# Kernel tuning notes

Measured on AMD Instinct MI355X. Metric: run time of the kernel, lower is better.

Reference implementation:

```python
import jax, jax.numpy as jnp
import numpy as np

K = 128          # num_clusters (init kwarg k)
N_ITERS = 100    # torch loop runs up to 100 iters; converged centroids are a
                 # fixed point, so running all 100 matches the early-exit result


def _sq_dists(x, c):
    # squared Euclidean distances [N, K]; argmin identical to torch.cdist argmin
    return (jnp.sum(x * x, axis=1, keepdims=True)
            - 2.0 * (x @ c.T)
            + jnp.sum(c * c, axis=1)[None, :])


def _assign_and_update(x, c):
    ids = jnp.argmin(_sq_dists(x, c), axis=1)                     # [N]
    sums = jax.ops.segment_sum(x, ids, num_segments=K)            # [K, D]
    counts = jax.ops.segment_sum(jnp.ones((x.shape[0],), x.dtype), ids,
                                 num_segments=K)                  # [K]
    return ids, sums / counts[:, None]   # mean per cluster (NaN if empty, as in torch)


def setup_inputs() -> dict:
    key = jax.random.key(0)
    kx, kp = jax.random.split(key)
    N, D = 32768, 256
    x = jax.random.normal(kx, (N, D), dtype=jnp.float32)
    # torch.randperm(N)[:K] -> distinct initial centroid indices
    init_idx = jax.random.permutation(kp, N)[:K].astype(jnp.int32)
    return {"x": x, "init_idx": init_idx}


def reference(x, init_idx):
    c0 = x[init_idx]  # [K, D]

    def body(c, _):
        _, newc = _assign_and_update(x, c)
        return newc, None

    # 99 updates, then final assignment + update: returned ids correspond to the
    # centroids BEFORE the last update, exactly like the torch loop's last iter.
    c, _ = jax.lax.scan(body, c0, None, length=N_ITERS - 1)
    ids, c = _assign_and_update(x, c)

    logits = x @ c.T  # temperature = 1.0
    logp = jax.nn.log_softmax(logits, axis=-1)
    # CrossEntropyLoss(mean) with pseudo labels = cluster ids
    loss = -jnp.mean(jnp.take_along_axis(logp, ids[:, None], axis=1))
    return loss
```

## Files before the change

kernel.cpp:

```cpp
#include <hip/hip_runtime.h>
#include <cstdint>

#define NPTS 32768
#define DIM  256
#define NK   128
#define NITER 100
#define NBLK 256
#define NTHR 1024
#define PAD  33

typedef unsigned short ushort_t;
typedef unsigned long long ull_t;
typedef __attribute__((ext_vector_type(8))) short s8v;
typedef __attribute__((ext_vector_type(4))) float f4v;

__device__ __forceinline__ unsigned short f2bf(float f) {
  unsigned u = __float_as_uint(f);
  u += 0x7fffu + ((u >> 16) & 1u);
  return (unsigned short)(u >> 16);
}
__device__ __forceinline__ float bf2f(unsigned short b) {
  return __uint_as_float(((unsigned)b) << 16);
}

__device__ __forceinline__ void cstore(float* p, float v) {
  __hip_atomic_store(p, v, __ATOMIC_RELAXED, __HIP_MEMORY_SCOPE_AGENT);
}
__device__ __forceinline__ float cload(const float* p) {
  return __hip_atomic_load(p, __ATOMIC_RELAXED, __HIP_MEMORY_SCOPE_AGENT);
}
__device__ __forceinline__ void cstorei(int* p, int v) {
  __hip_atomic_store(p, v, __ATOMIC_RELAXED, __HIP_MEMORY_SCOPE_AGENT);
}
__device__ __forceinline__ int cloadi(const int* p) {
  return __hip_atomic_load(p, __ATOMIC_RELAXED, __HIP_MEMORY_SCOPE_AGENT);
}
__device__ __forceinline__ void cstore64(ull_t* p, ull_t v) {
  __hip_atomic_store(p, v, __ATOMIC_RELAXED, __HIP_MEMORY_SCOPE_AGENT);
}
__device__ __forceinline__ f4v cload128f(const ull_t* p) {
  ull_t a = __hip_atomic_load(p, __ATOMIC_RELAXED, __HIP_MEMORY_SCOPE_AGENT);
  ull_t b = __hip_atomic_load(p + 1, __ATOMIC_RELAXED, __HIP_MEMORY_SCOPE_AGENT);
  f4v r;
  r[0] = __uint_as_float((unsigned)a); r[1] = __uint_as_float((unsigned)(a >> 32));
  r[2] = __uint_as_float((unsigned)b); r[3] = __uint_as_float((unsigned)(b >> 32));
  return r;
}

__device__ __forceinline__ void gbar(unsigned* flags, unsigned* grep, unsigned gen, bool inv) {
  __syncthreads();
  if (threadIdx.x == 0)
    __hip_atomic_store(&flags[blockIdx.x * 16], gen, __ATOMIC_RELAXED, __HIP_MEMORY_SCOPE_AGENT);
  if (blockIdx.x == 0) {
    if (threadIdx.x < NBLK) {
      while (__hip_atomic_load(&flags[threadIdx.x * 16], __ATOMIC_RELAXED, __HIP_MEMORY_SCOPE_AGENT) < gen)
        __builtin_amdgcn_s_sleep(2);
    }
    __syncthreads();
    if (threadIdx.x < 64)
      __hip_atomic_store(&grep[threadIdx.x * 16], gen, __ATOMIC_RELAXED, __HIP_MEMORY_SCOPE_AGENT);
  }
  if (threadIdx.x == 0) {
    while (__hip_atomic_load(&grep[(blockIdx.x & 63) * 16], __ATOMIC_RELAXED, __HIP_MEMORY_SCOPE_AGENT) < gen)
      __builtin_amdgcn_s_sleep(2);
  }
  __syncthreads();
  if (inv && threadIdx.x == 0) __threadfence();
  asm volatile("" ::: "memory");
  __syncthreads();
}

union StU {
  struct { char ch[128 * 80]; char cl[128 * 80]; } a;
  struct { float accB[NK * PAD]; ushort_t idsl16[1024]; } b;
  struct { float red4[1024]; float redcn[1024]; } c;
};

__device__ __forceinline__ void gemm_core(
    const s8v* __restrict__ xhR, const s8v* __restrict__ xlR,
    StU& u, float* cns, int t,
    const ull_t* __restrict__ cpk, const float* __restrict__ cn2, f4v (&acc)[2][2]) {
  const int lane = t & 63;
  const int w    = t >> 6;
  const int wr   = w >> 2, wc = w & 3;
  const int g    = lane >> 4, lr = lane & 15;

  if (t < NK) cns[t] = cload(&cn2[2 * t]) + cload(&cn2[2 * t + 1]);

  const f4v zero = {0.f, 0.f, 0.f, 0.f};
#pragma unroll
  for (int i = 0; i < 2; ++i)
#pragma unroll
    for (int j = 0; j < 2; ++j) acc[i][j] = zero;

  for (int q = 0; q < 8; ++q) {
    if (t < 512) {
      int row = t >> 2, c = t & 3;
      const ull_t* src = cpk + (size_t)row * 128 + q * 16 + c * 4;
      ull_t w0 = src[0], w1 = src[1], w2 = src[2], w3 = src[3];
      s8v vh, vl;
      vh[0] = (short)w0; vl[0] = (short)(w0 >> 16); vh[1] = (short)(w0 >> 32); vl[1] = (short)(w0 >> 48);
      vh[2] = (short)w1; vl[2] = (short)(w1 >> 16); vh[3] = (short)(w1 >> 32); vl[3] = (short)(w1 >> 48);
      vh[4] = (short)w2; vl[4] = (short)(w2 >> 16); vh[5] = (short)(w2 >> 32); vl[5] = (short)(w2 >> 48);
      vh[6] = (short)w3; vl[6] = (short)(w3 >> 16); vh[7] = (short)(w3 >> 32); vl[7] = (short)(w3 >> 48);
      *(s8v*)(u.a.ch + row * 80 + c * 16) = vh;
      *(s8v*)(u.a.cl + row * 80 + c * 16) = vl;
    }
    __syncthreads();
    s8v ah[2], al[2], bh[2], bl[2];
#pragma unroll
    for (int i = 0; i < 2; ++i) {
      int ra = wr * 32 + i * 16 + lr;
      int o = ra * 512 + (((q * 4 + g) ^ (lr & 7)) * 16);
      ah[i] = *(const s8v*)((const char*)xhR + o);
      al[i] = *(const s8v*)((const char*)xlR + o);
    }
#pragma unroll
    for (int j = 0; j < 2; ++j) {
      int rb = wc * 32 + j * 16 + lr;
      int o = rb * 80 + g * 16;
      bh[j] = *(const s8v*)(u.a.ch + o);
      bl[j] = *(const s8v*)(u.a.cl + o);
    }
#pragma unroll
    for (int i = 0; i < 2; ++i)
#pragma unroll
      for (int j = 0; j < 2; ++j) {
        acc[i][j] = __builtin_amdgcn_mfma_f32_16x16x32_bf16(ah[i], bh[j], acc[i][j], 0, 0, 0);
        acc[i][j] = __builtin_amdgcn_mfma_f32_16x16x32_bf16(ah[i], bl[j], acc[i][j], 0, 0, 0);
        acc[i][j] = __builtin_amdgcn_mfma_f32_16x16x32_bf16(al[i], bh[j], acc[i][j], 0, 0, 0);
      }
    __syncthreads();
  }
}

__global__ __launch_bounds__(NTHR, 1) void kmeans_fused(
    const float* __restrict__ x, const int* __restrict__ init_idx,
    ull_t* __restrict__ cpk, float* __restrict__ cn2, int* __restrict__ ids,
    float* __restrict__ psum, float* __restrict__ pcnt,
    float* __restrict__ outp, unsigned* __restrict__ flags,
    unsigned* __restrict__ grep, float* __restrict__ out) {
  __shared__ s8v xhR[4096];
  __shared__ s8v xlR[4096];
  __shared__ StU u;
  __shared__ float cns[NK];
  __shared__ float redd[NK * 4];
  __shared__ int   redk[NK * 4];
  __shared__ float gmaxs[NK];
  __shared__ float labvs[NK];
  __shared__ int   labis[NK];
  __shared__ int   cntB[NK];
  __shared__ ushort_t hsm[DIM], lsm[DIM];
  __shared__ float cntsh;

  const int b = blockIdx.x;
  const int t = threadIdx.x;
  const int lane = t & 63;
  const int w  = t >> 6;
  const int wr = w >> 2, wc = w & 3;
  const int g  = lane >> 4, lr = lane & 15;
  const int pbase = b * 128;
  unsigned gen = 1;

  for (int i = 0; i < 4; ++i) {
    int G = i * NTHR + t;
    int row = G >> 5, c = G & 31;
    const float4* src = (const float4*)(x + ((size_t)pbase + row) * DIM + c * 8);
    float4 fa = src[0], fb = src[1];
    float vv[8] = {fa.x, fa.y, fa.z, fa.w, fb.x, fb.y, fb.z, fb.w};
    s8v vh, vl;
#pragma unroll
    for (int j = 0; j < 8; ++j) {
      unsigned short hh = f2bf(vv[j]);
      vh[j] = (short)hh;
      vl[j] = (short)f2bf(vv[j] - bf2f(hh));
    }
    int pos = c ^ (row & 7);
    *(s8v*)((char*)xhR + row * 512 + pos * 16) = vh;
    *(s8v*)((char*)xlR + row * 512 + pos * 16) = vl;
  }

  if (b < NK) {
    float eff = 0.f;
    if (t < DIM) {
      float v = x[init_idx[b] * DIM + t];
      unsigned short hh = f2bf(v);
      unsigned short ll = f2bf(v - bf2f(hh));
      hsm[t] = hh; lsm[t] = ll;
      eff = bf2f(hh) + bf2f(ll);
    }
    __syncthreads();
    u.c.redcn[t] = (t < DIM) ? eff * eff : 0.f;
    if (t < NK) {
      ull_t wv = (ull_t)hsm[2 * t] | ((ull_t)lsm[2 * t] << 16)
               | ((ull_t)hsm[2 * t + 1] << 32) | ((ull_t)lsm[2 * t + 1] << 48);
      cstore64(&cpk[(size_t)b * 128 + t], wv);
    }
    __syncthreads();
    for (int s = 512; s > 0; s >>= 1) { if (t < s) u.c.redcn[t] += u.c.redcn[t + s]; __syncthreads(); }
    if (t == 0) { cstore(&cn2[b * 2], u.c.redcn[0]); cstore(&cn2[b * 2 + 1], 0.f); }
  }
  gbar(flags, grep, gen, true); ++gen;

  for (int it = 0; it < NITER; ++it) {
    {
      f4v acc[2][2];
      gemm_core(xhR, xlR, u, cns, t, cpk, cn2, acc);
#pragma unroll
      for (int i = 0; i < 2; ++i) {
#pragma unroll
        for (int r = 0; r < 4; ++r) {
          int prow = wr * 32 + i * 16 + g * 4 + r;
          float bd = 1e30f; int bk = 0;
#pragma unroll
          for (int j = 0; j < 2; ++j) {
            int col = wc * 32 + j * 16 + lr;
            float s = cns[col] - 2.f * acc[i][j][r];
            if (s < bd || (s == bd && col < bk)) { bd = s; bk = col; }
          }
#pragma unroll
          for (int msk = 1; msk < 16; msk <<= 1) {
            float od = __shfl_xor(bd, msk, 64);
            int   ok = __shfl_xor(bk, msk, 64);
            if (od < bd || (od == bd && ok < bk)) { bd = od; bk = ok; }
          }
          if (lr == 0) { redd[prow * 4 + wc] = bd; redk[prow * 4 + wc] = bk; }
        }
      }
      __syncthreads();
      if (t < NK) {
        float bd = redd[t * 4]; int bk = redk[t * 4];
#pragma unroll
        for (int q = 1; q < 4; ++q) {
          float dq = redd[t * 4 + q]; int kq = redk[t * 4 + q];
          if (dq < bd || (dq == bd && kq < bk)) { bd = dq; bk = kq; }
        }
        cstorei(&ids[pbase + t], bk);
      }
    }
    gbar(flags, grep, gen, false); ++gen;

    {
      const int pg = b & 31, dg = b >> 5;
      for (int i = t; i < NK * PAD; i += NTHR) u.b.accB[i] = 0.f;
      if (t < NK) cntB[t] = 0;
      u.b.idsl16[t] = (ushort_t)cloadi(&ids[pg * 1024 + t]);
      __syncthreads();
      const int id = u.b.idsl16[t];
      if (dg == 0) atomicAdd(&cntB[id], 1);
      const ull_t* xr = (const ull_t*)(x + ((size_t)pg * 1024 + t) * DIM + dg * 32);
      f4v v0 = cload128f(xr + 0),  v1 = cload128f(xr + 2);
      f4v v2 = cload128f(xr + 4),  v3 = cload128f(xr + 6);
      f4v v4 = cload128f(xr + 8),  v5 = cload128f(xr + 10);
      f4v v6 = cload128f(xr + 12), v7 = cload128f(xr + 14);
      float* ab = &u.b.accB[id * PAD];
      atomicAdd(ab + 0,  v0[0]); atomicAdd(ab + 1,  v0[1]); atomicAdd(ab + 2,  v0[2]); atomicAdd(ab + 3,  v0[3]);
      atomicAdd(ab + 4,  v1[0]); atomicAdd(ab + 5,  v1[1]); atomicAdd(ab + 6,  v1[2]); atomicAdd(ab + 7,  v1[3]);
      atomicAdd(ab + 8,  v2[0]); atomicAdd(ab + 9,  v2[1]); atomicAdd(ab + 10, v2[2]); atomicAdd(ab + 11, v2[3]);
      atomicAdd(ab + 12, v3[0]); atomicAdd(ab + 13, v3[1]); atomicAdd(ab + 14, v3[2]); atomicAdd(ab + 15, v3[3]);
      atomicAdd(ab + 16, v4[0]); atomicAdd(ab + 17, v4[1]); atomicAdd(ab + 18, v4[2]); atomicAdd(ab + 19, v4[3]);
      atomicAdd(ab + 20, v5[0]); atomicAdd(ab + 21, v5[1]); atomicAdd(ab + 22, v5[2]); atomicAdd(ab + 23, v5[3]);
      atomicAdd(ab + 24, v6[0]); atomicAdd(ab + 25, v6[1]); atomicAdd(ab + 26, v6[2]); atomicAdd(ab + 27, v6[3]);
      atomicAdd(ab + 28, v7[0]); atomicAdd(ab + 29, v7[1]); atomicAdd(ab + 30, v7[2]); atomicAdd(ab + 31, v7[3]);
      __syncthreads();
#pragma unroll
      for (int s2 = 0; s2 < 4; ++s2) {
        int idx = s2 * NTHR + t;
        int k2 = idx >> 5, dl = idx & 31;
        cstore(&psum[(((size_t)dg * NK + k2) * 32 + pg) * 32 + dl], u.b.accB[k2 * PAD + dl]);
      }
      if (dg == 0 && t < NK)
        cstore(&pcnt[(size_t)pg * NK + t], (float)cntB[t]);
    }
    gbar(flags, grep, gen, false); ++gen;

    {
      const int k = b >> 1, hh2 = b & 1;
      const int dwh = t & 127, pch = t >> 7;
      const int dgc = hh2 * 4 + (dwh >> 5), dlc = dwh & 31;
      float s = 0.f;
#pragma unroll
      for (int p2 = pch * 4; p2 < pch * 4 + 4; ++p2)
        s += cload(&psum[(((size_t)dgc * NK + k) * 32 + p2) * 32 + dlc]);
      u.c.red4[pch * 128 + dwh] = s;
      float cv = (t < 32) ? cload(&pcnt[(size_t)t * NK + k]) : 0.f;
      if (t < 64) {
#pragma unroll
        for (int m = 1; m < 32; m <<= 1) cv += __shfl_xor(cv, m, 64);
      }
      if (t == 0) cntsh = cv;
      __syncthreads();
      float eff = 0.f;
      if (t < 128) {
        float ssum = 0.f;
#pragma unroll
        for (int ww = 0; ww < 8; ++ww) ssum += u.c.red4[ww * 128 + t];
        float mean = ssum / cntsh;
        unsigned short hh = f2bf(mean);
        unsigned short ll = f2bf(mean - bf2f(hh));
        hsm[t] = hh; lsm[t] = ll;
        eff = bf2f(hh) + bf2f(ll);
      }
      __syncthreads();
      u.c.redcn[t] = (t < 128) ? eff * eff : 0.f;
      if (t < 64) {
        ull_t wv = (ull_t)hsm[2 * t] | ((ull_t)lsm[2 * t] << 16)
                 | ((ull_t)hsm[2 * t + 1] << 32) | ((ull_t)lsm[2 * t + 1] << 48);
        cstore64(&cpk[(size_t)k * 128 + hh2 * 64 + t], wv);
      }
      __syncthreads();
      for (int st = 512; st > 0; st >>= 1) { if (t < st) u.c.redcn[t] += u.c.redcn[t + st]; __syncthreads(); }
      if (t == 0) cstore(&cn2[k * 2 + hh2], u.c.redcn[0]);
    }
    gbar(flags, grep, gen, true); ++gen;
  }

  {
    f4v acc[2][2];
    gemm_core(xhR, xlR, u, cns, t, cpk, cn2, acc);
#pragma unroll
    for (int i = 0; i < 2; ++i) {
#pragma unroll
      for (int r = 0; r < 4; ++r) {
        int prow = wr * 32 + i * 16 + g * 4 + r;
        float m = -1e30f;
#pragma unroll
        for (int j = 0; j < 2; ++j) m = fmaxf(m, acc[i][j][r]);
#pragma unroll
        for (int msk = 1; msk < 16; msk <<= 1) m = fmaxf(m, __shfl_xor(m, msk, 64));
        if (lr == 0) redd[prow * 4 + wc] = m;
      }
    }
    __syncthreads();
    if (t < NK) {
      float m = redd[t * 4];
#pragma unroll
      for (int q = 1; q < 4; ++q) m = fmaxf(m, redd[t * 4 + q]);
      gmaxs[t] = m;
      labis[t] = cloadi(&ids[pbase + t]);
    }
    __syncthreads();
#pragma unroll
    for (int i = 0; i < 2; ++i) {
#pragma unroll
      for (int r = 0; r < 4; ++r) {
        int prow = wr * 32 + i * 16 + g * 4 + r;
        float m = gmaxs[prow];
        int lab = labis[prow];
        float s = 0.f;
#pragma unroll
        for (int j = 0; j < 2; ++j) {
          int col = wc * 32 + j * 16 + lr;
          float v = acc[i][j][r];
          s += expf(v - m);
          if (col == lab) labvs[prow] = v;
        }
#pragma unroll
        for (int msk = 1; msk < 16; msk <<= 1) s += __shfl_xor(s, msk, 64);
        if (lr == 0) redd[prow * 4 + wc] = s;
      }
    }
    __syncthreads();
    if (t < NK) {
      float se = redd[t * 4] + redd[t * 4 + 1] + redd[t * 4 + 2] + redd[t * 4 + 3];
      float lse = gmaxs[t] + logf(se);
      gmaxs[t] = lse - labvs[t];
    }
    __syncthreads();
    if (t == 0) {
      float tot = 0.f;
      for (int q = 0; q < NK; ++q) tot += gmaxs[q];
      cstore(&outp[b], tot);
    }
  }
  gbar(flags, grep, gen, false); ++gen;
  if (b == 0) {
    u.c.redcn[t] = (t < NBLK) ? cload(&outp[t]) : 0.f;
    __syncthreads();
    for (int s = 512; s > 0; s >>= 1) { if (t < s) u.c.redcn[t] += u.c.redcn[t + s]; __syncthreads(); }
    if (t == 0) out[0] = u.c.redcn[0] * (1.0f / (float)NPTS);
  }
}

extern "C" void kernel_launch(void* const* d_in, const int* in_sizes, int n_in,
                              void* d_out, int out_size, void* d_ws, size_t ws_size,
                              hipStream_t stream) {
  const float* x        = (const float*)d_in[0];
  const int*   init_idx = (const int*)d_in[1];
  float* out = (float*)d_out;
  char* ws = (char*)d_ws;

  ull_t* cpk  = (ull_t*)(ws);
  float* cn2  = (float*)(ws + 131072);
  int*   ids  = (int*)(ws + 132096);
  float* psum = (float*)(ws + 263168);
  float* pcnt = (float*)(ws + 4457472);
  float* outp = (float*)(ws + 4473856);
  unsigned* flags = (unsigned*)(ws + 4474880);
  unsigned* grep  = (unsigned*)(ws + 4491264);

  hipMemsetAsync(flags, 0, 20480, stream);
  kmeans_fused<<<dim3(NBLK), dim3(NTHR), 0, stream>>>(
      x, init_idx, cpk, cn2, ids, psum, pcnt, outp, flags, grep, out);
}
```

Baseline: 7.192 ms.

## Version centroid buffers per iteration to drop per-iteration cache invalidation fences

Centroids and their norms are now written to a fresh workspace slot each iteration (101 versions), so readers never see stale cached copies of an address they read before. This lets the global barrier drop its per-iteration threadfence invalidation, keeping only one fence after the init barrier. The x loads in the update phase also become plain float4 loads instead of paired atomic 64-bit loads, since x is read-only. The cost is a much larger workspace (about 13 MB of centroid history), and correctness now depends on the cache-coherence assumption that never-read addresses miss to memory.

```diff
diff --git a/kernel.cpp b/kernel.cpp
--- a/kernel.cpp
+++ b/kernel.cpp
@@ -38,16 +38,8 @@
 __device__ __forceinline__ void cstore64(ull_t* p, ull_t v) {
   __hip_atomic_store(p, v, __ATOMIC_RELAXED, __HIP_MEMORY_SCOPE_AGENT);
 }
-__device__ __forceinline__ f4v cload128f(const ull_t* p) {
-  ull_t a = __hip_atomic_load(p, __ATOMIC_RELAXED, __HIP_MEMORY_SCOPE_AGENT);
-  ull_t b = __hip_atomic_load(p + 1, __ATOMIC_RELAXED, __HIP_MEMORY_SCOPE_AGENT);
-  f4v r;
-  r[0] = __uint_as_float((unsigned)a); r[1] = __uint_as_float((unsigned)(a >> 32));
-  r[2] = __uint_as_float((unsigned)b); r[3] = __uint_as_float((unsigned)(b >> 32));
-  return r;
-}
-
-__device__ __forceinline__ void gbar(unsigned* flags, unsigned* grep, unsigned gen, bool inv) {
+
+__device__ __forceinline__ void gbar(unsigned* flags, unsigned* grep, unsigned gen) {
   __syncthreads();
   if (threadIdx.x == 0)
     __hip_atomic_store(&flags[blockIdx.x * 16], gen, __ATOMIC_RELAXED, __HIP_MEMORY_SCOPE_AGENT);
@@ -65,7 +57,6 @@
       __builtin_amdgcn_s_sleep(2);
   }
   __syncthreads();
-  if (inv && threadIdx.x == 0) __threadfence();
   asm volatile("" ::: "memory");
   __syncthreads();
 }
@@ -136,7 +127,7 @@
 
 __global__ __launch_bounds__(NTHR, 1) void kmeans_fused(
     const float* __restrict__ x, const int* __restrict__ init_idx,
-    ull_t* __restrict__ cpk, float* __restrict__ cn2, int* __restrict__ ids,
+    ull_t* __restrict__ cpkv, float* __restrict__ cn2v, int* __restrict__ ids,
     float* __restrict__ psum, float* __restrict__ pcnt,
     float* __restrict__ outp, unsigned* __restrict__ flags,
     unsigned* __restrict__ grep, float* __restrict__ out) {
@@ -194,18 +185,25 @@
     if (t < NK) {
       ull_t wv = (ull_t)hsm[2 * t] | ((ull_t)lsm[2 * t] << 16)
                | ((ull_t)hsm[2 * t + 1] << 32) | ((ull_t)lsm[2 * t + 1] << 48);
-      cstore64(&cpk[(size_t)b * 128 + t], wv);
+      cstore64(&cpkv[(size_t)b * 128 + t], wv);
     }
     __syncthreads();
     for (int s = 512; s > 0; s >>= 1) { if (t < s) u.c.redcn[t] += u.c.redcn[t + s]; __syncthreads(); }
-    if (t == 0) { cstore(&cn2[b * 2], u.c.redcn[0]); cstore(&cn2[b * 2 + 1], 0.f); }
-  }
-  gbar(flags, grep, gen, true); ++gen;
+    if (t == 0) { cstore(&cn2v[b * 2], u.c.redcn[0]); cstore(&cn2v[b * 2 + 1], 0.f); }
+  }
+  gbar(flags, grep, gen); ++gen;
+  if (t == 0) __threadfence();
+  __syncthreads();
 
   for (int it = 0; it < NITER; ++it) {
+    const ull_t*  cpkR = cpkv + (size_t)it * (NK * 128);
+    const float*  cn2R = cn2v + (size_t)it * (NK * 2);
+    ull_t* cpkW = cpkv + (size_t)(it + 1) * (NK * 128);
+    float* cn2W = cn2v + (size_t)(it + 1) * (NK * 2);
+
     {
       f4v acc[2][2];
-      gemm_core(xhR, xlR, u, cns, t, cpk, cn2, acc);
+      gemm_core(xhR, xlR, u, cns, t, cpkR, cn2R, acc);
 #pragma unroll
       for (int i = 0; i < 2; ++i) {
 #pragma unroll
@@ -238,7 +236,7 @@
         cstorei(&ids[pbase + t], bk);
       }
     }
-    gbar(flags, grep, gen, false); ++gen;
+    gbar(flags, grep, gen); ++gen;
 
     {
       const int pg = b & 31, dg = b >> 5;
@@ -248,20 +246,18 @@
       __syncthreads();
       const int id = u.b.idsl16[t];
       if (dg == 0) atomicAdd(&cntB[id], 1);
-      const ull_t* xr = (const ull_t*)(x + ((size_t)pg * 1024 + t) * DIM + dg * 32);
-      f4v v0 = cload128f(xr + 0),  v1 = cload128f(xr + 2);
-      f4v v2 = cload128f(xr + 4),  v3 = cload128f(xr + 6);
-      f4v v4 = cload128f(xr + 8),  v5 = cload128f(xr + 10);
-      f4v v6 = cload128f(xr + 12), v7 = cload128f(xr + 14);
+      const float4* xr = (const float4*)(x + ((size_t)pg * 1024 + t) * DIM + dg * 32);
+      float4 v0 = xr[0], v1 = xr[1], v2 = xr[2], v3 = xr[3];
+      float4 v4 = xr[4], v5 = xr[5], v6 = xr[6], v7 = xr[7];
       float* ab = &u.b.accB[id * PAD];
-      atomicAdd(ab + 0,  v0[0]); atomicAdd(ab + 1,  v0[1]); atomicAdd(ab + 2,  v0[2]); atomicAdd(ab + 3,  v0[3]);
-      atomicAdd(ab + 4,  v1[0]); atomicAdd(ab + 5,  v1[1]); atomicAdd(ab + 6,  v1[2]); atomicAdd(ab + 7,  v1[3]);
-      atomicAdd(ab + 8,  v2[0]); atomicAdd(ab + 9,  v2[1]); atomicAdd(ab + 10, v2[2]); atomicAdd(ab + 11, v2[3]);
-      atomicAdd(ab + 12, v3[0]); atomicAdd(ab + 13, v3[1]); atomicAdd(ab + 14, v3[2]); atomicAdd(ab + 15, v3[3]);
-      atomicAdd(ab + 16, v4[0]); atomicAdd(ab + 17, v4[1]); atomicAdd(ab + 18, v4[2]); atomicAdd(ab + 19, v4[3]);
-      atomicAdd(ab + 20, v5[0]); atomicAdd(ab + 21, v5[1]); atomicAdd(ab + 22, v5[2]); atomicAdd(ab + 23, v5[3]);
-      atomicAdd(ab + 24, v6[0]); atomicAdd(ab + 25, v6[1]); atomicAdd(ab + 26, v6[2]); atomicAdd(ab + 27, v6[3]);
-      atomicAdd(ab + 28, v7[0]); atomicAdd(ab + 29, v7[1]); atomicAdd(ab + 30, v7[2]); atomicAdd(ab + 31, v7[3]);
+      atomicAdd(ab + 0,  v0.x); atomicAdd(ab + 1,  v0.y); atomicAdd(ab + 2,  v0.z); atomicAdd(ab + 3,  v0.w);
+      atomicAdd(ab + 4,  v1.x); atomicAdd(ab + 5,  v1.y); atomicAdd(ab + 6,  v1.z); atomicAdd(ab + 7,  v1.w);
+      atomicAdd(ab + 8,  v2.x); atomicAdd(ab + 9,  v2.y); atomicAdd(ab + 10, v2.z); atomicAdd(ab + 11, v2.w);
+      atomicAdd(ab + 12, v3.x); atomicAdd(ab + 13, v3.y); atomicAdd(ab + 14, v3.z); atomicAdd(ab + 15, v3.w);
+      atomicAdd(ab + 16, v4.x); atomicAdd(ab + 17, v4.y); atomicAdd(ab + 18, v4.z); atomicAdd(ab + 19, v4.w);
+      atomicAdd(ab + 20, v5.x); atomicAdd(ab + 21, v5.y); atomicAdd(ab + 22, v5.z); atomicAdd(ab + 23, v5.w);
+      atomicAdd(ab + 24, v6.x); atomicAdd(ab + 25, v6.y); atomicAdd(ab + 26, v6.z); atomicAdd(ab + 27, v6.w);
+      atomicAdd(ab + 28, v7.x); atomicAdd(ab + 29, v7.y); atomicAdd(ab + 30, v7.z); atomicAdd(ab + 31, v7.w);
       __syncthreads();
 #pragma unroll
       for (int s2 = 0; s2 < 4; ++s2) {
@@ -272,7 +268,7 @@
       if (dg == 0 && t < NK)
         cstore(&pcnt[(size_t)pg * NK + t], (float)cntB[t]);
     }
-    gbar(flags, grep, gen, false); ++gen;
+    gbar(flags, grep, gen); ++gen;
 
     {
       const int k = b >> 1, hh2 = b & 1;
@@ -306,18 +302,19 @@
       if (t < 64) {
         ull_t wv = (ull_t)hsm[2 * t] | ((ull_t)lsm[2 * t] << 16)
                  | ((ull_t)hsm[2 * t + 1] << 32) | ((ull_t)lsm[2 * t + 1] << 48);
-        cstore64(&cpk[(size_t)k * 128 + hh2 * 64 + t], wv);
+        cstore64(&cpkW[(size_t)k * 128 + hh2 * 64 + t], wv);
       }
       __syncthreads();
       for (int st = 512; st > 0; st >>= 1) { if (t < st) u.c.redcn[t] += u.c.redcn[t + st]; __syncthreads(); }
-      if (t == 0) cstore(&cn2[k * 2 + hh2], u.c.redcn[0]);
-    }
-    gbar(flags, grep, gen, true); ++gen;
+      if (t == 0) cstore(&cn2W[k * 2 + hh2], u.c.redcn[0]);
+    }
+    gbar(flags, grep, gen); ++gen;
   }
 
   {
     f4v acc[2][2];
-    gemm_core(xhR, xlR, u, cns, t, cpk, cn2, acc);
+    gemm_core(xhR, xlR, u, cns, t,
+              cpkv + (size_t)NITER * (NK * 128), cn2v + (size_t)NITER * (NK * 2), acc);
 #pragma unroll
     for (int i = 0; i < 2; ++i) {
 #pragma unroll
@@ -373,7 +370,7 @@
       cstore(&outp[b], tot);
     }
   }
-  gbar(flags, grep, gen, false); ++gen;
+  gbar(flags, grep, gen); ++gen;
   if (b == 0) {
     u.c.redcn[t] = (t < NBLK) ? cload(&outp[t]) : 0.f;
     __syncthreads();
@@ -390,16 +387,16 @@
   float* out = (float*)d_out;
   char* ws = (char*)d_ws;
 
-  ull_t* cpk  = (ull_t*)(ws);
-  float* cn2  = (float*)(ws + 131072);
-  int*   ids  = (int*)(ws + 132096);
-  float* psum = (float*)(ws + 263168);
-  float* pcnt = (float*)(ws + 4457472);
-  float* outp = (float*)(ws + 4473856);
-  unsigned* flags = (unsigned*)(ws + 4474880);
-  unsigned* grep  = (unsigned*)(ws + 4491264);
+  ull_t* cpkv = (ull_t*)(ws);
+  float* cn2v = (float*)(ws + 13238272);
+  int*   ids  = (int*)(ws + 13341696);
+  float* psum = (float*)(ws + 13472768);
+  float* pcnt = (float*)(ws + 17667072);
+  float* outp = (float*)(ws + 17683456);
+  unsigned* flags = (unsigned*)(ws + 17684480);
+  unsigned* grep  = (unsigned*)(ws + 17700864);
 
   hipMemsetAsync(flags, 0, 20480, stream);
   kmeans_fused<<<dim3(NBLK), dim3(NTHR), 0, stream>>>(
-      x, init_idx, cpk, cn2, ids, psum, pcnt, outp, flags, grep, out);
-}
+      x, init_idx, cpkv, cn2v, ids, psum, pcnt, outp, flags, grep, out);
+}
```

Result: faster. 6.861 ms, median of 2 (-4.6%).
